# Performance work log

Hardware: AMD Instinct MI355X
Metric: run time of the kernel (lower is better)

Reference implementation:

```python
import jax, jax.numpy as jnp
import numpy as np

N_NODES = 100000
EMB = 16
HID = 64
N_EDGES = 4194304


def setup_inputs() -> dict:
    key = jax.random.key(0)
    k_emb, k_e, k1, k2, k3 = jax.random.split(key, 5)
    node_embeddings = jax.random.normal(k_emb, (N_NODES, EMB), dtype=jnp.float32)
    edge_index = jax.random.randint(k_e, (2, N_EDGES), 0, N_NODES, dtype=jnp.int32)
    # MLP params: Linear(2*EMB -> HID), Linear(HID -> HID//2), Linear(HID//2 -> 1)
    s1 = 1.0 / np.sqrt(2 * EMB)
    s2 = 1.0 / np.sqrt(HID)
    s3 = 1.0 / np.sqrt(HID // 2)
    W1 = jax.random.uniform(k1, (2 * EMB, HID), jnp.float32, -s1, s1)
    b1 = jnp.zeros((HID,), jnp.float32)
    W2 = jax.random.uniform(k2, (HID, HID // 2), jnp.float32, -s2, s2)
    b2 = jnp.zeros((HID // 2,), jnp.float32)
    W3 = jax.random.uniform(k3, (HID // 2, 1), jnp.float32, -s3, s3)
    b3 = jnp.zeros((1,), jnp.float32)
    return {"node_embeddings": node_embeddings, "edge_index": edge_index,
            "W1": W1, "b1": b1, "W2": W2, "b2": b2, "W3": W3, "b3": b3}


def reference(node_embeddings, edge_index, W1, b1, W2, b2, W3, b3):
    # Gather node-pair embeddings and concat: [E, 2*EMB]
    feats = jnp.concatenate([node_embeddings[edge_index[0]],
                             node_embeddings[edge_index[1]]], axis=1)
    # 3-layer MLP (dropout is identity in eval mode)
    h = jax.nn.relu(feats @ W1 + b1)
    h = jax.nn.relu(h @ W2 + b2)
    edge_probs = jax.nn.sigmoid(h @ W3 + b3)  # [E, 1]
    return edge_probs, edge_index
```

## Files before the change

kernel.cpp:

```cpp
#include <hip/hip_runtime.h>
#include <hip/hip_bf16.h>

#define NEMB 16

typedef short s16x8 __attribute__((ext_vector_type(8)));
typedef float f32x16 __attribute__((ext_vector_type(16)));

__device__ __forceinline__ unsigned int pack_bf16x2_rnd(float lo, float hi) {
    unsigned int ul = __float_as_uint(lo);
    unsigned int uh = __float_as_uint(hi);
    return ((ul + 0x8000u) >> 16) | ((uh + 0x8000u) & 0xffff0000u);
}
__device__ __forceinline__ unsigned int pack_bf16x2_trunc(float lo, float hi) {
    return __builtin_amdgcn_perm(__float_as_uint(hi), __float_as_uint(lo),
                                 0x07060302u);
}

__global__ __launch_bounds__(256) void emb_to_bf16_kernel(
        const float* __restrict__ emb, unsigned int* __restrict__ embT,
        int nWords) {
    int i = (blockIdx.x * 256 + threadIdx.x) * 4;
    if (i + 4 <= nWords) {
        float4 a = *reinterpret_cast<const float4*>(emb + 2 * i);
        float4 b = *reinterpret_cast<const float4*>(emb + 2 * i + 4);
        uint4 r;
        r.x = pack_bf16x2_rnd(a.x, a.y);
        r.y = pack_bf16x2_rnd(a.z, a.w);
        r.z = pack_bf16x2_rnd(b.x, b.y);
        r.w = pack_bf16x2_rnd(b.z, b.w);
        *reinterpret_cast<uint4*>(embT + i) = r;
    } else {
        for (; i < nWords; ++i)
            embT[i] = pack_bf16x2_rnd(emb[2 * i], emb[2 * i + 1]);
    }
}

#define WAVES 4
#define ITERS 8
#define EDGES_PER_BLOCK (WAVES * 32 * ITERS)

__global__ __launch_bounds__(256) void edge_fused4_kernel(
        const unsigned short* __restrict__ embT,
        const int* __restrict__ ei,
        const float* __restrict__ W1, const float* __restrict__ b1,
        const float* __restrict__ W2, const float* __restrict__ b2,
        const float* __restrict__ W3, const float* __restrict__ b3,
        float* __restrict__ out, int nE) {
    const int tid = threadIdx.x;
    const int w  = tid >> 6;
    const int l  = tid & 63;
    const int el = l & 31;
    const int hi = l >> 5;

    s16x8 A1[2][2];
#pragma unroll
    for (int jt = 0; jt < 2; ++jt)
#pragma unroll
        for (int kh = 0; kh < 2; ++kh) {
            s16x8 a;
#pragma unroll
            for (int i = 0; i < 8; ++i) {
                float v = W1[(kh * 16 + hi * 8 + i) * 64 + jt * 32 + el];
                a[i] = (short)((__float_as_uint(v) + 0x8000u) >> 16);
            }
            A1[jt][kh] = a;
        }
    s16x8 A2[4];
#pragma unroll
    for (int f = 0; f < 4; ++f) {
        s16x8 a;
#pragma unroll
        for (int i = 0; i < 8; ++i) {
            float v = W2[(f * 16 + hi * 8 + i) * 32 + el];
            a[i] = (short)((__float_as_uint(v) + 0x8000u) >> 16);
        }
        A2[f] = a;
    }
    f32x16 b1v0, b1v1, b2v;
    float w3v[16];
#pragma unroll
    for (int r = 0; r < 16; ++r) {
        int n = (r & 3) + 8 * (r >> 2) + 4 * hi;
        b1v0[r] = b1[n];
        b1v1[r] = b1[32 + n];
        b2v[r]  = b2[n];
        w3v[r]  = W3[n];
    }
    const float b3v = b3[0];

    const int base0 = blockIdx.x * EDGES_PER_BLOCK + w * 32;

    int sv[ITERS], dv[ITERS];
#pragma unroll
    for (int i = 0; i < ITERS; ++i) {
        int e  = base0 + i * (WAVES * 32) + el;
        int ec = e < nE ? e : (nE - 1);
        sv[i] = ei[ec];
        dv[i] = ei[nE + ec];
    }

    auto GATHER = [&](int s, int d, uint4& es, uint4& ed) {
        es = *reinterpret_cast<const uint4*>(embT + ((size_t)s << 4) + (hi << 3));
        ed = *reinterpret_cast<const uint4*>(embT + ((size_t)d << 4) + (hi << 3));
    };

    auto DO_TILE = [&](uint4 esq, uint4 edq, int it, int s, int d) {
        union { uint4 q; s16x8 v; } es, edr;
        es.q = esq; edr.q = edq;

        __builtin_amdgcn_s_setprio(1);
        f32x16 a0 = __builtin_amdgcn_mfma_f32_32x32x16_bf16(A1[0][0], es.v,  b1v0, 0, 0, 0);
        a0        = __builtin_amdgcn_mfma_f32_32x32x16_bf16(A1[0][1], edr.v, a0,   0, 0, 0);
        f32x16 a1 = __builtin_amdgcn_mfma_f32_32x32x16_bf16(A1[1][0], es.v,  b1v1, 0, 0, 0);
        a1        = __builtin_amdgcn_mfma_f32_32x32x16_bf16(A1[1][1], edr.v, a1,   0, 0, 0);

        union { unsigned int u[4]; s16x8 v; } bf0, bf1, bf2, bf3;
#define MAKE_FRAG(BF, AT, M)                                                   \
        {                                                                      \
            unsigned int x0 = pack_bf16x2_trunc(fmaxf((AT)[8*(M)+0], 0.f),     \
                                                fmaxf((AT)[8*(M)+1], 0.f));    \
            unsigned int x1 = pack_bf16x2_trunc(fmaxf((AT)[8*(M)+2], 0.f),     \
                                                fmaxf((AT)[8*(M)+3], 0.f));    \
            unsigned int y0 = pack_bf16x2_trunc(fmaxf((AT)[8*(M)+4], 0.f),     \
                                                fmaxf((AT)[8*(M)+5], 0.f));    \
            unsigned int y1 = pack_bf16x2_trunc(fmaxf((AT)[8*(M)+6], 0.f),     \
                                                fmaxf((AT)[8*(M)+7], 0.f));    \
            asm("v_permlane32_swap_b32 %0, %1" : "+v"(x0), "+v"(y0));          \
            asm("v_permlane32_swap_b32 %0, %1" : "+v"(x1), "+v"(y1));          \
            BF.u[0] = x0; BF.u[1] = x1; BF.u[2] = y0; BF.u[3] = y1;            \
        }
        MAKE_FRAG(bf0, a0, 0)
        MAKE_FRAG(bf1, a0, 1)
        MAKE_FRAG(bf2, a1, 0)
        MAKE_FRAG(bf3, a1, 1)
#undef MAKE_FRAG

        f32x16 acc;
        acc = __builtin_amdgcn_mfma_f32_32x32x16_bf16(A2[0], bf0.v, b2v, 0, 0, 0);
        acc = __builtin_amdgcn_mfma_f32_32x32x16_bf16(A2[1], bf1.v, acc, 0, 0, 0);
        acc = __builtin_amdgcn_mfma_f32_32x32x16_bf16(A2[2], bf2.v, acc, 0, 0, 0);
        acc = __builtin_amdgcn_mfma_f32_32x32x16_bf16(A2[3], bf3.v, acc, 0, 0, 0);
        __builtin_amdgcn_s_setprio(0);

        float pr[16];
#pragma unroll
        for (int r = 0; r < 16; ++r)
            pr[r] = fmaxf(acc[r], 0.0f) * w3v[r];
        float s8[8];
#pragma unroll
        for (int r = 0; r < 8; ++r) s8[r] = pr[2 * r] + pr[2 * r + 1];
        float s4[4];
#pragma unroll
        for (int r = 0; r < 4; ++r) s4[r] = s8[2 * r] + s8[2 * r + 1];
        float v = (s4[0] + s4[1]) + (s4[2] + s4[3]);
        {
            float va = v, vb = v;
            asm("v_permlane32_swap_b32 %0, %1" : "+v"(vb), "+v"(va));
            v = va + vb;
        }

        float p = 1.0f / (1.0f + __expf(-(v + b3v)));

        int e = base0 + it * (WAVES * 32) + el;
        if (e < nE) {
            if (hi == 0) {
                out[e] = p;
                out[nE + e] = (float)s;
            } else {
                out[(size_t)2 * nE + e] = (float)d;
            }
        }
    };

    uint4 esX, edX, esY, edY, esZ, edZ;
    GATHER(sv[0], dv[0], esX, edX);
    GATHER(sv[1], dv[1], esY, edY);

    GATHER(sv[2], dv[2], esZ, edZ);  DO_TILE(esX, edX, 0, sv[0], dv[0]);
    GATHER(sv[3], dv[3], esX, edX);  DO_TILE(esY, edY, 1, sv[1], dv[1]);
    GATHER(sv[4], dv[4], esY, edY);  DO_TILE(esZ, edZ, 2, sv[2], dv[2]);
    GATHER(sv[5], dv[5], esZ, edZ);  DO_TILE(esX, edX, 3, sv[3], dv[3]);
    GATHER(sv[6], dv[6], esX, edX);  DO_TILE(esY, edY, 4, sv[4], dv[4]);
    GATHER(sv[7], dv[7], esY, edY);  DO_TILE(esZ, edZ, 5, sv[5], dv[5]);
    DO_TILE(esX, edX, 6, sv[6], dv[6]);
    DO_TILE(esY, edY, 7, sv[7], dv[7]);
}

__global__ __launch_bounds__(256) void edge_mlp_naive_kernel(
        const float* __restrict__ emb, const int* __restrict__ ei,
        const float* __restrict__ W1, const float* __restrict__ b1,
        const float* __restrict__ W2, const float* __restrict__ b2,
        const float* __restrict__ W3, const float* __restrict__ b3,
        float* __restrict__ out, int nE) {
    __shared__ __align__(16) float sW1[32 * 64];
    __shared__ __align__(16) float sW2[64 * 32];
    __shared__ float sW3[32];
    __shared__ float sB1[64];
    __shared__ float sB2[32];
    __shared__ float sB3;
    for (int i = threadIdx.x; i < 2048; i += 256) {
        sW1[i] = W1[i];
        sW2[i] = W2[i];
    }
    if (threadIdx.x < 64) sB1[threadIdx.x] = b1[threadIdx.x];
    if (threadIdx.x < 32) {
        sW3[threadIdx.x] = W3[threadIdx.x];
        sB2[threadIdx.x] = b2[threadIdx.x];
    }
    if (threadIdx.x == 0) sB3 = b3[0];
    __syncthreads();

    int e = blockIdx.x * 256 + threadIdx.x;
    if (e >= nE) return;

    int s = ei[e];
    int d = ei[nE + e];

    float f[32];
    const float4* ps = reinterpret_cast<const float4*>(emb + (size_t)s * NEMB);
    const float4* pd = reinterpret_cast<const float4*>(emb + (size_t)d * NEMB);
#pragma unroll
    for (int q = 0; q < 4; ++q) {
        float4 v = ps[q];
        f[4 * q + 0] = v.x; f[4 * q + 1] = v.y; f[4 * q + 2] = v.z; f[4 * q + 3] = v.w;
    }
#pragma unroll
    for (int q = 0; q < 4; ++q) {
        float4 v = pd[q];
        f[16 + 4 * q + 0] = v.x; f[16 + 4 * q + 1] = v.y;
        f[16 + 4 * q + 2] = v.z; f[16 + 4 * q + 3] = v.w;
    }

    float h1[64];
#pragma unroll
    for (int j = 0; j < 64; j += 4) {
        float a0 = sB1[j + 0], a1 = sB1[j + 1], a2 = sB1[j + 2], a3 = sB1[j + 3];
#pragma unroll
        for (int k = 0; k < 32; ++k) {
            float4 wv = *reinterpret_cast<const float4*>(sW1 + k * 64 + j);
            a0 = fmaf(f[k], wv.x, a0);
            a1 = fmaf(f[k], wv.y, a1);
            a2 = fmaf(f[k], wv.z, a2);
            a3 = fmaf(f[k], wv.w, a3);
        }
        h1[j + 0] = fmaxf(a0, 0.0f);
        h1[j + 1] = fmaxf(a1, 0.0f);
        h1[j + 2] = fmaxf(a2, 0.0f);
        h1[j + 3] = fmaxf(a3, 0.0f);
    }

    float acc = sB3;
#pragma unroll
    for (int j = 0; j < 32; j += 4) {
        float a0 = sB2[j + 0], a1 = sB2[j + 1], a2 = sB2[j + 2], a3 = sB2[j + 3];
#pragma unroll
        for (int k = 0; k < 64; ++k) {
            float4 wv = *reinterpret_cast<const float4*>(sW2 + k * 32 + j);
            a0 = fmaf(h1[k], wv.x, a0);
            a1 = fmaf(h1[k], wv.y, a1);
            a2 = fmaf(h1[k], wv.z, a2);
            a3 = fmaf(h1[k], wv.w, a3);
        }
        acc = fmaf(fmaxf(a0, 0.0f), sW3[j + 0], acc);
        acc = fmaf(fmaxf(a1, 0.0f), sW3[j + 1], acc);
        acc = fmaf(fmaxf(a2, 0.0f), sW3[j + 2], acc);
        acc = fmaf(fmaxf(a3, 0.0f), sW3[j + 3], acc);
    }

    out[e] = 1.0f / (1.0f + __expf(-acc));
}

__global__ __launch_bounds__(256) void edge_idx_copy_kernel(
        const int* __restrict__ ei, float* __restrict__ out, int n) {
    int i = (blockIdx.x * 256 + threadIdx.x) * 4;
    if (i + 4 <= n) {
        int4 a = *reinterpret_cast<const int4*>(ei + i);
        float4 r = make_float4((float)a.x, (float)a.y, (float)a.z, (float)a.w);
        *reinterpret_cast<float4*>(out + i) = r;
    } else {
        for (; i < n; ++i) out[i] = (float)ei[i];
    }
}

extern "C" void kernel_launch(void* const* d_in, const int* in_sizes, int n_in,
                              void* d_out, int out_size, void* d_ws, size_t ws_size,
                              hipStream_t stream) {
    const float* emb = (const float*)d_in[0];
    const int*   ei  = (const int*)d_in[1];
    const float* W1  = (const float*)d_in[2];
    const float* b1  = (const float*)d_in[3];
    const float* W2  = (const float*)d_in[4];
    const float* b2  = (const float*)d_in[5];
    const float* W3  = (const float*)d_in[6];
    const float* b3  = (const float*)d_in[7];

    const int nNodes = in_sizes[0] / NEMB;
    const int n2E    = in_sizes[1];
    const int nE     = n2E / 2;

    float* out = (float*)d_out;

    const size_t tbl_bytes = (size_t)nNodes * NEMB * sizeof(unsigned short);
    const bool use_ws = (ws_size >= tbl_bytes);

    if (use_ws) {
        unsigned int* embT = (unsigned int*)d_ws;
        const int nWords = nNodes * 8;
        emb_to_bf16_kernel<<<(nWords / 4 + 255) / 256, 256, 0, stream>>>(
            emb, embT, nWords);

        edge_fused4_kernel<<<(nE + EDGES_PER_BLOCK - 1) / EDGES_PER_BLOCK, 256, 0,
                             stream>>>(
            (const unsigned short*)embT, ei, W1, b1, W2, b2, W3, b3, out, nE);
    } else {
        edge_mlp_naive_kernel<<<(nE + 255) / 256, 256, 0, stream>>>(
            emb, ei, W1, b1, W2, b2, W3, b3, out, nE);
        edge_idx_copy_kernel<<<((n2E + 3) / 4 + 255) / 256, 256, 0, stream>>>(
            ei, out + nE, n2E);
    }
}
```

Before: 87.75 us.

## Compute final MLP layer with MFMA and shorten gather prefetch depth

Replaces the scalar layer-3 dot product (per-lane multiply, tree reduction, permlane swap) with two bf16 MFMA instructions, after repacking the ReLU'd layer-2 output into bf16 fragments. Bias b3 is folded into the accumulator init. The gather prefetch is also reduced from a three-buffer to a two-buffer ping-pong loop. This trades VALU reduction work for extra MFMA work and bf16 truncation of the hidden activations. It also lowers how much gather latency is hidden, which may save registers.

```diff
diff --git a/kernel.cpp b/kernel.cpp
--- a/kernel.cpp
+++ b/kernel.cpp
@@ -39,7 +39,7 @@
 #define ITERS 8
 #define EDGES_PER_BLOCK (WAVES * 32 * ITERS)
 
-__global__ __launch_bounds__(256) void edge_fused4_kernel(
+__global__ __launch_bounds__(256) void edge_fused5_kernel(
         const unsigned short* __restrict__ embT,
         const int* __restrict__ ei,
         const float* __restrict__ W1, const float* __restrict__ b1,
@@ -76,17 +76,27 @@
         }
         A2[f] = a;
     }
-    f32x16 b1v0, b1v1, b2v;
-    float w3v[16];
+    s16x8 A3[2];
+#pragma unroll
+    for (int f3 = 0; f3 < 2; ++f3) {
+        s16x8 a;
+#pragma unroll
+        for (int i = 0; i < 8; ++i) {
+            float v = W3[f3 * 16 + hi * 8 + i];
+            a[i] = (short)((__float_as_uint(v) + 0x8000u) >> 16);
+        }
+        A3[f3] = a;
+    }
+    f32x16 b1v0, b1v1, b2v, C3;
+    const float b3v = b3[0];
 #pragma unroll
     for (int r = 0; r < 16; ++r) {
         int n = (r & 3) + 8 * (r >> 2) + 4 * hi;
         b1v0[r] = b1[n];
         b1v1[r] = b1[32 + n];
         b2v[r]  = b2[n];
-        w3v[r]  = W3[n];
-    }
-    const float b3v = b3[0];
+        C3[r]   = b3v;
+    }
 
     const int base0 = blockIdx.x * EDGES_PER_BLOCK + w * 32;
 
@@ -133,33 +143,23 @@
         MAKE_FRAG(bf1, a0, 1)
         MAKE_FRAG(bf2, a1, 0)
         MAKE_FRAG(bf3, a1, 1)
-#undef MAKE_FRAG
 
         f32x16 acc;
         acc = __builtin_amdgcn_mfma_f32_32x32x16_bf16(A2[0], bf0.v, b2v, 0, 0, 0);
         acc = __builtin_amdgcn_mfma_f32_32x32x16_bf16(A2[1], bf1.v, acc, 0, 0, 0);
         acc = __builtin_amdgcn_mfma_f32_32x32x16_bf16(A2[2], bf2.v, acc, 0, 0, 0);
         acc = __builtin_amdgcn_mfma_f32_32x32x16_bf16(A2[3], bf3.v, acc, 0, 0, 0);
+
+        union { unsigned int u[4]; s16x8 v; } cf0, cf1;
+        MAKE_FRAG(cf0, acc, 0)
+        MAKE_FRAG(cf1, acc, 1)
+#undef MAKE_FRAG
+        f32x16 acc3;
+        acc3 = __builtin_amdgcn_mfma_f32_32x32x16_bf16(A3[0], cf0.v, C3,   0, 0, 0);
+        acc3 = __builtin_amdgcn_mfma_f32_32x32x16_bf16(A3[1], cf1.v, acc3, 0, 0, 0);
         __builtin_amdgcn_s_setprio(0);
 
-        float pr[16];
-#pragma unroll
-        for (int r = 0; r < 16; ++r)
-            pr[r] = fmaxf(acc[r], 0.0f) * w3v[r];
-        float s8[8];
-#pragma unroll
-        for (int r = 0; r < 8; ++r) s8[r] = pr[2 * r] + pr[2 * r + 1];
-        float s4[4];
-#pragma unroll
-        for (int r = 0; r < 4; ++r) s4[r] = s8[2 * r] + s8[2 * r + 1];
-        float v = (s4[0] + s4[1]) + (s4[2] + s4[3]);
-        {
-            float va = v, vb = v;
-            asm("v_permlane32_swap_b32 %0, %1" : "+v"(vb), "+v"(va));
-            v = va + vb;
-        }
-
-        float p = 1.0f / (1.0f + __expf(-(v + b3v)));
+        float p = 1.0f / (1.0f + __expf(-acc3[0]));
 
         int e = base0 + it * (WAVES * 32) + el;
         if (e < nE) {
@@ -172,18 +172,15 @@
         }
     };
 
-    uint4 esX, edX, esY, edY, esZ, edZ;
-    GATHER(sv[0], dv[0], esX, edX);
-    GATHER(sv[1], dv[1], esY, edY);
-
-    GATHER(sv[2], dv[2], esZ, edZ);  DO_TILE(esX, edX, 0, sv[0], dv[0]);
-    GATHER(sv[3], dv[3], esX, edX);  DO_TILE(esY, edY, 1, sv[1], dv[1]);
-    GATHER(sv[4], dv[4], esY, edY);  DO_TILE(esZ, edZ, 2, sv[2], dv[2]);
-    GATHER(sv[5], dv[5], esZ, edZ);  DO_TILE(esX, edX, 3, sv[3], dv[3]);
-    GATHER(sv[6], dv[6], esX, edX);  DO_TILE(esY, edY, 4, sv[4], dv[4]);
-    GATHER(sv[7], dv[7], esY, edY);  DO_TILE(esZ, edZ, 5, sv[5], dv[5]);
-    DO_TILE(esX, edX, 6, sv[6], dv[6]);
-    DO_TILE(esY, edY, 7, sv[7], dv[7]);
+    uint4 esA, edA, esB, edB;
+    GATHER(sv[0], dv[0], esA, edA);
+#pragma unroll
+    for (int it = 0; it < ITERS; it += 2) {
+        if (it + 1 < ITERS) GATHER(sv[it + 1], dv[it + 1], esB, edB);
+        DO_TILE(esA, edA, it, sv[it], dv[it]);
+        if (it + 2 < ITERS) GATHER(sv[it + 2], dv[it + 2], esA, edA);
+        if (it + 1 < ITERS) DO_TILE(esB, edB, it + 1, sv[it + 1], dv[it + 1]);
+    }
 }
 
 __global__ __launch_bounds__(256) void edge_mlp_naive_kernel(
@@ -309,7 +306,7 @@
         emb_to_bf16_kernel<<<(nWords / 4 + 255) / 256, 256, 0, stream>>>(
             emb, embT, nWords);
 
-        edge_fused4_kernel<<<(nE + EDGES_PER_BLOCK - 1) / EDGES_PER_BLOCK, 256, 0,
+        edge_fused5_kernel<<<(nE + EDGES_PER_BLOCK - 1) / EDGES_PER_BLOCK, 256, 0,
                              stream>>>(
             (const unsigned short*)embT, ei, W1, b1, W2, b2, W3, b3, out, nE);
     } else {
```

Result: slower. 101.6 us (+15.8%).
